# Kernel optimization log

Measured on AMD Instinct MI355X. Metric: run time of the kernel, lower is better.

Reference implementation:

```python
import jax, jax.numpy as jnp
import numpy as np

B, T, I, H = 256, 2048, 128, 128


def setup_inputs() -> dict:
    key = jax.random.key(0)
    ks = jax.random.split(key, 20)
    stdv = 1.0 / float(np.sqrt(H))
    u = lambda k, shape: jax.random.uniform(k, shape, jnp.float32, -stdv, stdv)
    return {
        "inputs": jax.random.normal(ks[0], (B, T, I), jnp.float32),
        "h": jax.random.normal(ks[1], (1, 1, H), jnp.float32),
        "c": jax.random.normal(ks[2], (1, H), jnp.float32),
        "w_ii": u(ks[3], (1, I, H)), "w_hi": u(ks[4], (1, H, H)),
        "b_ii": u(ks[5], (1, 1, H)), "b_hi": u(ks[6], (1, 1, H)),
        "w_if": u(ks[7], (1, I, H)), "w_hf": u(ks[8], (1, H, H)),
        "b_if": u(ks[9], (1, H)),    "b_hf": u(ks[10], (1, H)),
        "w_io": u(ks[11], (1, I, H)), "w_ho": u(ks[12], (1, H, H)),
        "b_io": u(ks[13], (1, 1, H)), "b_ho": u(ks[14], (1, 1, H)),
        "w_ig": u(ks[15], (1, I, H)), "w_hg": u(ks[16], (1, H, H)),
        "b_ig": u(ks[17], (1, 1, H)), "b_hg": u(ks[18], (1, 1, H)),
    }


def reference(inputs, h, c,
              w_ii, w_hi, b_ii, b_hi,
              w_if, w_hf, b_if, b_hf,
              w_io, w_ho, b_io, b_ho,
              w_ig, w_hg, b_ig, b_hg):
    # Faithful to the source: h_t and c_t are NEVER updated inside the time
    # loop (only h_next_t/c_next_t are stored), so every timestep uses the
    # initial state and the whole sequence vectorizes into one batched pass.
    h_t = h.reshape(1, -1)            # h.squeeze(0): (1, H)
    Hd = h_t.shape[-1]

    def gate(w_i, b_i, w_h, b_h):
        # inputs:(B,T,I) @ w_i[0]:(I,H) -> (B,T,H); state term constant over t
        return (jnp.einsum('bti,ih->bth', inputs, w_i[0])
                + b_i.reshape(1, 1, Hd)
                + (h_t @ w_h[0]).reshape(1, 1, Hd)
                + b_h.reshape(1, 1, Hd))

    i = jax.nn.sigmoid(gate(w_ii, b_ii, w_hi, b_hi))
    f = jax.nn.sigmoid(gate(w_if, b_if, w_hf, b_hf))
    g = jnp.tanh(gate(w_ig, b_ig, w_hg, b_hg))
    o = jax.nn.sigmoid(gate(w_io, b_io, w_ho, b_ho))

    c_next = f * c.reshape(1, 1, Hd) + i * g      # (B,T,H)
    h_next = o * jnp.tanh(c_next)                 # (B,T,H)

    hidden_seq = jnp.transpose(h_next, (1, 0, 2))[:, :, None, :]  # (T,B,1,H)
    h_last = h_next[:, -1, :][:, None, :]         # (B,1,H)
    c_last = c_next[:, -1, :][:, None, :]         # (B,1,H)
    return hidden_seq, h_last, c_last
```

## Files before the change

kernel.cpp:

```cpp
#include <hip/hip_runtime.h>


typedef __attribute__((ext_vector_type(8))) short short8;
typedef __attribute__((ext_vector_type(4))) float f32x4;
typedef __attribute__((ext_vector_type(2))) unsigned int uint2v;

#define GRID  512
#define THREADS 512
#define CHUNK 32
#define M_    524288
#define ITERS 32
#define LSTR  272
#define AB0   0
#define AB1   (32 * LSTR)
#define OB    (2 * 32 * LSTR)
#define LSTRO 528
#define LDSSZ (OB + 32 * LSTRO)

__device__ __forceinline__ unsigned fbits(float f) {
    union { float f; unsigned u; } v; v.f = f; return v.u;
}
__device__ __forceinline__ unsigned short f2bf(float f) {
    unsigned u = fbits(f);
    return (unsigned short)((u + 0x7FFFu + ((u >> 16) & 1u)) >> 16);
}
__device__ __forceinline__ unsigned packbf2(float a, float b) {
    unsigned ua = fbits(a) , ub = fbits(b);
    ua = ua + 0x7FFFu + ((ua >> 16) & 1u);
    ub = ub + 0x7FFFu + ((ub >> 16) & 1u);
    return (ub & 0xFFFF0000u) | (ua >> 16);
}
__device__ __forceinline__ float clamp30(float x) {
    return fminf(fmaxf(x, -30.f), 30.f);
}

__global__ __launch_bounds__(THREADS, 4)
void lstm_main(const float* __restrict__ x,
               const float* __restrict__ h0,
               const float* __restrict__ c0,
               const float* __restrict__ wi0, const float* __restrict__ wh0,
               const float* __restrict__ bi0, const float* __restrict__ bh0,
               const float* __restrict__ wi1, const float* __restrict__ wh1,
               const float* __restrict__ bi1, const float* __restrict__ bh1,
               const float* __restrict__ wi2, const float* __restrict__ wh2,
               const float* __restrict__ bi2, const float* __restrict__ bh2,
               const float* __restrict__ wi3, const float* __restrict__ wh3,
               const float* __restrict__ bi3, const float* __restrict__ bh3,
               float* __restrict__ out)
{
    __shared__ __align__(16) char lds[LDSSZ];
    const int tid  = threadIdx.x;
    const int ww   = tid >> 6;
    const int lane = tid & 63;
    const int lo   = lane & 15;
    const int hi   = lane >> 4;
    const int col  = ww * 16 + lo;

    float* sbuf = (float*)(lds + OB);
    {
        const int pc = tid & 127;
        const int g  = tid >> 7;
        const float* wh = (g == 0) ? wh0 : (g == 1) ? wh1 : (g == 2) ? wh2 : wh3;
        const float* bi = (g == 0) ? bi0 : (g == 1) ? bi1 : (g == 2) ? bi2 : bi3;
        const float* bh = (g == 0) ? bh0 : (g == 1) ? bh1 : (g == 2) ? bh2 : bh3;
        float a = bi[pc] + bh[pc];
        #pragma unroll 8
        for (int k = 0; k < 128; ++k)
            a += h0[k] * wh[k * 128 + pc];
        sbuf[g * 128 + pc] = a;
    }
    __syncthreads();

    float sv[4], c0v;
    #pragma unroll
    for (int g = 0; g < 4; ++g) sv[g] = sbuf[g * 128 + col];
    c0v = c0[col];

    short8 Bf[4][4];
    {
        const float* Wi[4] = { wi0, wi1, wi2, wi3 };
        #pragma unroll
        for (int g = 0; g < 4; ++g) {
            #pragma unroll
            for (int kt = 0; kt < 4; ++kt) {
                short8 v;
                #pragma unroll
                for (int j = 0; j < 8; ++j)
                    v[j] = (short)f2bf(Wi[g][(kt * 32 + hi * 8 + j) * 128 + col]);
                Bf[g][kt] = v;
            }
        }
    }

    const float4* xv4 = (const float4*)x;
    int m0 = blockIdx.x * CHUNK;
    {
        #pragma unroll
        for (int j = 0; j < 2; ++j) {
            const int f = j * 512 + tid;
            float4 v = xv4[m0 * 32 + f];
            uint2v p;
            p.x = packbf2(v.x, v.y);
            p.y = packbf2(v.z, v.w);
            *(uint2v*)(lds + AB0 + (f >> 5) * LSTR + (f & 31) * 8) = p;
        }
    }
    __syncthreads();

    float* hseq  = out;
    float* hlast = out + 67108864;
    float* clast = out + 67108864 + 32768;

    for (int it = 0; it < ITERS; ++it) {
        const char* Ab = lds + ((it & 1) ? AB1 : AB0);

        float4 pf[2];
        if (it + 1 < ITERS) {
            const int m0n = m0 + GRID * CHUNK;
            #pragma unroll
            for (int j = 0; j < 2; ++j)
                pf[j] = xv4[m0n * 32 + j * 512 + tid];
        }

        f32x4 acc[2][4];
        #pragma unroll
        for (int mt = 0; mt < 2; ++mt)
            #pragma unroll
            for (int g = 0; g < 4; ++g)
                acc[mt][g] = (f32x4){0.f, 0.f, 0.f, 0.f};

        #pragma unroll
        for (int kt = 0; kt < 4; ++kt) {
            short8 a0 = *(const short8*)(Ab + lo * LSTR + (kt * 4 + hi) * 16);
            short8 a1 = *(const short8*)(Ab + (16 + lo) * LSTR + (kt * 4 + hi) * 16);
            #pragma unroll
            for (int g = 0; g < 4; ++g) {
                acc[0][g] = __builtin_amdgcn_mfma_f32_16x16x32_bf16(a0, Bf[g][kt], acc[0][g], 0, 0, 0);
                acc[1][g] = __builtin_amdgcn_mfma_f32_16x16x32_bf16(a1, Bf[g][kt], acc[1][g], 0, 0, 0);
            }
        }

        const bool lastChunk = ((m0 & 2047) == 2016);
        const int  b = m0 >> 11;
        const float K1 = 1.44269504f, K2 = 2.88539008f;
        #pragma unroll
        for (int mt = 0; mt < 2; ++mt) {
            #pragma unroll
            for (int reg = 0; reg < 4; ++reg) {
                float ai = clamp30(acc[mt][0][reg] + sv[0]);
                float af = clamp30(acc[mt][1][reg] + sv[1]);
                float ao = clamp30(acc[mt][2][reg] + sv[2]);
                float ag = clamp30(acc[mt][3][reg] + sv[3]);
                float ti = __builtin_amdgcn_exp2f(-K1 * ai);
                float tf = __builtin_amdgcn_exp2f(-K1 * af);
                float to = __builtin_amdgcn_exp2f(-K1 * ao);
                float tg = __builtin_amdgcn_exp2f(-K2 * ag);
                float fg = __builtin_amdgcn_rcpf(1.f + tf);
                float ig = (1.f - tg) * __builtin_amdgcn_rcpf((1.f + ti) * (1.f + tg));
                float cv = clamp30(fg * c0v + ig);
                float tc = __builtin_amdgcn_exp2f(-K2 * cv);
                float hv = (1.f - tc) * __builtin_amdgcn_rcpf((1.f + to) * (1.f + tc));
                const int r = mt * 16 + hi * 4 + reg;
                *(float*)(lds + OB + r * LSTRO + col * 4) = hv;
                if (lastChunk && mt == 1 && reg == 3 && hi == 3)
                    clast[b * 128 + col] = cv;
            }
        }

        if (it + 1 < ITERS) {
            char* An = lds + ((it & 1) ? AB0 : AB1);
            #pragma unroll
            for (int j = 0; j < 2; ++j) {
                const int f = j * 512 + tid;
                uint2v p;
                p.x = packbf2(pf[j].x, pf[j].y);
                p.y = packbf2(pf[j].z, pf[j].w);
                *(uint2v*)(An + (f >> 5) * LSTR + (f & 31) * 8) = p;
            }
        }
        __syncthreads();

        #pragma unroll
        for (int j = 0; j < 2; ++j) {
            const int f = j * 512 + tid;
            const int r = f >> 5;
            const int c = f & 31;
            float4 vv = *(const float4*)(lds + OB + r * LSTRO + c * 16);
            const int m = m0 + r;
            const int t = m & 2047;
            *(float4*)(hseq + (t * 256 + b) * 128 + c * 4) = vv;
            if (t == 2047)
                *(float4*)(hlast + b * 128 + c * 4) = vv;
        }
        __syncthreads();

        m0 += GRID * CHUNK;
    }
}

extern "C" void kernel_launch(void* const* d_in, const int* in_sizes, int n_in,
                              void* d_out, int out_size, void* d_ws, size_t ws_size,
                              hipStream_t stream) {
    (void)in_sizes; (void)n_in; (void)out_size; (void)d_ws; (void)ws_size;
    const float* x  = (const float*)d_in[0];
    const float* h0 = (const float*)d_in[1];
    const float* c0 = (const float*)d_in[2];
    lstm_main<<<dim3(GRID), dim3(THREADS), 0, stream>>>(
        x, h0, c0,
        (const float*)d_in[3],  (const float*)d_in[4],
        (const float*)d_in[5],  (const float*)d_in[6],
        (const float*)d_in[7],  (const float*)d_in[8],
        (const float*)d_in[9],  (const float*)d_in[10],
        (const float*)d_in[11], (const float*)d_in[12],
        (const float*)d_in[13], (const float*)d_in[14],
        (const float*)d_in[15], (const float*)d_in[16],
        (const float*)d_in[17], (const float*)d_in[18],
        (float*)d_out);
}
```

Baseline: 505.1 us.

## Write hidden outputs directly from MFMA registers and use hardware bf16 conversion

Drops the LDS staging of h values and the extra barrier plus float4 copy-out. Each lane now stores its scalar h result straight to global memory. Manual round-to-nearest bf16 packing is replaced by the v_cvt_pk_bf16_f32 instruction, and the clamp uses fmed3. The direct stores are 4-byte writes, each quarter-wave covering 64 contiguous bytes, in place of 16-byte vector stores, so global write coalescing may get worse in exchange for less LDS traffic and synchronisation.

```diff
diff --git a/kernel.cpp b/kernel.cpp
--- a/kernel.cpp
+++ b/kernel.cpp
@@ -13,25 +13,16 @@
 #define LSTR  272
 #define AB0   0
 #define AB1   (32 * LSTR)
-#define OB    (2 * 32 * LSTR)
-#define LSTRO 528
-#define LDSSZ (OB + 32 * LSTRO)
-
-__device__ __forceinline__ unsigned fbits(float f) {
-    union { float f; unsigned u; } v; v.f = f; return v.u;
-}
-__device__ __forceinline__ unsigned short f2bf(float f) {
-    unsigned u = fbits(f);
-    return (unsigned short)((u + 0x7FFFu + ((u >> 16) & 1u)) >> 16);
-}
-__device__ __forceinline__ unsigned packbf2(float a, float b) {
-    unsigned ua = fbits(a) , ub = fbits(b);
-    ua = ua + 0x7FFFu + ((ua >> 16) & 1u);
-    ub = ub + 0x7FFFu + ((ub >> 16) & 1u);
-    return (ub & 0xFFFF0000u) | (ua >> 16);
+#define SB    (2 * 32 * LSTR)
+#define LDSSZ (SB + 2048)
+
+__device__ __forceinline__ unsigned cvtpk(float a, float b) {
+    unsigned r;
+    asm("v_cvt_pk_bf16_f32 %0, %1, %2" : "=v"(r) : "v"(a), "v"(b));
+    return r;
 }
 __device__ __forceinline__ float clamp30(float x) {
-    return fminf(fmaxf(x, -30.f), 30.f);
+    return __builtin_amdgcn_fmed3f(x, -30.f, 30.f);
 }
 
 __global__ __launch_bounds__(THREADS, 4)
@@ -56,7 +47,7 @@
     const int hi   = lane >> 4;
     const int col  = ww * 16 + lo;
 
-    float* sbuf = (float*)(lds + OB);
+    float* sbuf = (float*)(lds + SB);
     {
         const int pc = tid & 127;
         const int g  = tid >> 7;
@@ -83,11 +74,12 @@
         for (int g = 0; g < 4; ++g) {
             #pragma unroll
             for (int kt = 0; kt < 4; ++kt) {
-                short8 v;
+                const float* wp = Wi[g] + (kt * 32 + hi * 8) * 128 + col;
+                union { unsigned u[4]; short8 s; } v;
                 #pragma unroll
-                for (int j = 0; j < 8; ++j)
-                    v[j] = (short)f2bf(Wi[g][(kt * 32 + hi * 8 + j) * 128 + col]);
-                Bf[g][kt] = v;
+                for (int j = 0; j < 4; ++j)
+                    v.u[j] = cvtpk(wp[(2 * j) * 128], wp[(2 * j + 1) * 128]);
+                Bf[g][kt] = v.s;
             }
         }
     }
@@ -100,8 +92,8 @@
             const int f = j * 512 + tid;
             float4 v = xv4[m0 * 32 + f];
             uint2v p;
-            p.x = packbf2(v.x, v.y);
-            p.y = packbf2(v.z, v.w);
+            p.x = cvtpk(v.x, v.y);
+            p.y = cvtpk(v.z, v.w);
             *(uint2v*)(lds + AB0 + (f >> 5) * LSTR + (f & 31) * 8) = p;
         }
     }
@@ -140,8 +132,10 @@
             }
         }
 
-        const bool lastChunk = ((m0 & 2047) == 2016);
-        const int  b = m0 >> 11;
+        const int  t0 = m0 & 2047;
+        const int  b  = m0 >> 11;
+        const bool lastChunk = (t0 == 2016);
+        float* hp = hseq + (size_t)(t0 * 256 + b) * 128 + (size_t)hi * 4 * 32768 + col;
         const float K1 = 1.44269504f, K2 = 2.88539008f;
         #pragma unroll
         for (int mt = 0; mt < 2; ++mt) {
@@ -160,10 +154,11 @@
                 float cv = clamp30(fg * c0v + ig);
                 float tc = __builtin_amdgcn_exp2f(-K2 * cv);
                 float hv = (1.f - tc) * __builtin_amdgcn_rcpf((1.f + to) * (1.f + tc));
-                const int r = mt * 16 + hi * 4 + reg;
-                *(float*)(lds + OB + r * LSTRO + col * 4) = hv;
-                if (lastChunk && mt == 1 && reg == 3 && hi == 3)
+                hp[(size_t)(mt * 16 + reg) * 32768] = hv;
+                if (lastChunk && mt == 1 && reg == 3 && hi == 3) {
+                    hlast[b * 128 + col] = hv;
                     clast[b * 128 + col] = cv;
+                }
             }
         }
 
@@ -173,24 +168,10 @@
             for (int j = 0; j < 2; ++j) {
                 const int f = j * 512 + tid;
                 uint2v p;
-                p.x = packbf2(pf[j].x, pf[j].y);
-                p.y = packbf2(pf[j].z, pf[j].w);
+                p.x = cvtpk(pf[j].x, pf[j].y);
+                p.y = cvtpk(pf[j].z, pf[j].w);
                 *(uint2v*)(An + (f >> 5) * LSTR + (f & 31) * 8) = p;
             }
-        }
-        __syncthreads();
-
-        #pragma unroll
-        for (int j = 0; j < 2; ++j) {
-            const int f = j * 512 + tid;
-            const int r = f >> 5;
-            const int c = f & 31;
-            float4 vv = *(const float4*)(lds + OB + r * LSTRO + c * 16);
-            const int m = m0 + r;
-            const int t = m & 2047;
-            *(float4*)(hseq + (t * 256 + b) * 128 + c * 4) = vv;
-            if (t == 2047)
-                *(float4*)(hlast + b * 128 + c * 4) = vv;
         }
         __syncthreads();
 
```

New measurement: 509.6 us. No clear change (+0.9%).
